# Optimization experiments

Measured on AMD Instinct MI355X. Metric: run time of the kernel, lower is better.

The kernel has to match this reference:

```python
import jax, jax.numpy as jnp
import numpy as np

N_NODES = 30000
N_EDGES = 480000
N_GRAPHS = 500
D_IN = 78


def gcn_conv(x, W, b, src, dst, n_nodes):
    """PyG GCNConv: add self-loops, sym-normalize, linear then aggregate, bias after."""
    xw = x @ W  # [N, d_out]
    deg = jnp.zeros((n_nodes,), x.dtype).at[dst].add(1.0) + 1.0  # +1 self-loop
    dinv = jax.lax.rsqrt(deg)
    norm = dinv[src] * dinv[dst]  # [E]
    msg = xw[src] * norm[:, None]  # [E, d_out] edge gather
    out = jnp.zeros_like(xw).at[dst].add(msg)  # scatter-add to dst
    out = out + xw * (dinv * dinv)[:, None]  # self-loop contribution
    return out + b


def setup_inputs() -> dict:
    key = jax.random.key(0)
    ks = jax.random.split(key, 16)
    x = jax.random.normal(ks[0], (N_NODES, D_IN), dtype=jnp.float32)
    edge_index = jax.random.randint(ks[1], (2, N_EDGES), 0, N_NODES, dtype=jnp.int32)
    batch = jnp.sort(jax.random.randint(ks[2], (N_NODES,), 0, N_GRAPHS, dtype=jnp.int32))

    def lin(k, fi, fo):
        s = 1.0 / np.sqrt(fi)
        k1, k2 = jax.random.split(k)
        W = jax.random.uniform(k1, (fi, fo), jnp.float32, -s, s)
        b = jax.random.uniform(k2, (fo,), jnp.float32, -s, s)
        return W, b

    W1, b1 = lin(ks[3], D_IN, D_IN)
    W2, b2 = lin(ks[4], D_IN, D_IN * 2)
    W3, b3 = lin(ks[5], D_IN * 2, D_IN * 4)
    Wf1, bf1 = lin(ks[6], D_IN * 4, 1024)
    Wf2, bf2 = lin(ks[7], 1024, 128)
    return {"x": x, "edge_index": edge_index, "batch": batch,
            "W1": W1, "b1": b1, "W2": W2, "b2": b2, "W3": W3, "b3": b3,
            "Wf1": Wf1, "bf1": bf1, "Wf2": Wf2, "bf2": bf2}


def reference(x, edge_index, batch, W1, b1, W2, b2, W3, b3, Wf1, bf1, Wf2, bf2):
    src, dst = edge_index[0], edge_index[1]
    n = x.shape[0]
    h = jax.nn.relu(gcn_conv(x, W1, b1, src, dst, n))
    h = jax.nn.relu(gcn_conv(h, W2, b2, src, dst, n))
    h = jax.nn.relu(gcn_conv(h, W3, b3, src, dst, n))
    # global max pool over graphs
    pooled = jax.ops.segment_max(h, batch, num_segments=N_GRAPHS)  # [G, 312]
    pooled = jnp.where(jnp.isfinite(pooled), pooled, 0.0)  # guard empty segments
    out = jax.nn.relu(pooled @ Wf1 + bf1)
    out = out @ Wf2 + bf2  # dropout is identity in eval mode
    return out
```

## Files before the change

kernel.cpp:

```cpp
#include <hip/hip_runtime.h>

#define NODES  30000
#define EDGES  480000
#define GRAPHS 500
#define MPAD   30016
#define NB     118

typedef __bf16 bf16x8 __attribute__((ext_vector_type(8)));
typedef float  f32x4  __attribute__((ext_vector_type(4)));

__device__ __forceinline__ float4 f4add(float4 a, float4 b) {
    a.x += b.x; a.y += b.y; a.z += b.z; a.w += b.w; return a;
}

__device__ __forceinline__ void split_f32(float a, unsigned short& hi, unsigned short& lo) {
    unsigned int u = __float_as_uint(a);
    unsigned int rh = (u + 0x7fffu + ((u >> 16) & 1u)) & 0xffff0000u;
    hi = (unsigned short)(rh >> 16);
    float l = a - __uint_as_float(rh);
    unsigned int ul = __float_as_uint(l);
    lo = (unsigned short)((ul + 0x7fffu + ((ul >> 16) & 1u)) >> 16);
}

__device__ __forceinline__ void gload_lds16(const void* g, void* l) {
    __builtin_amdgcn_global_load_lds(
        (__attribute__((address_space(1))) void*)g,
        (__attribute__((address_space(3))) void*)l, 16, 0, 0);
}

__global__ void count_kernel(const int* __restrict__ dst, int* __restrict__ cnt, int E) {
    int i = blockIdx.x * blockDim.x + threadIdx.x;
    if (i < E) atomicAdd(&cnt[dst[i]], 1);
}

__global__ __launch_bounds__(256) void scan_bsum_kernel(const int* __restrict__ cnt,
                                                        int* __restrict__ bsum, int n) {
    __shared__ int buf[256];
    int t = threadIdx.x;
    int i = blockIdx.x * 256 + t;
    buf[t] = (i < n) ? cnt[i] : 0;
    __syncthreads();
    for (int ofs = 128; ofs > 0; ofs >>= 1) {
        if (t < ofs) buf[t] += buf[t + ofs];
        __syncthreads();
    }
    if (t == 0) bsum[blockIdx.x] = buf[0];
}

__global__ __launch_bounds__(128) void scan_top_kernel(const int* __restrict__ bsum,
                                                       int* __restrict__ boff) {
    __shared__ int buf[128];
    int t = threadIdx.x;
    int own = (t < NB) ? bsum[t] : 0;
    buf[t] = own;
    __syncthreads();
    for (int ofs = 1; ofs < 128; ofs <<= 1) {
        int v = (t >= ofs) ? buf[t - ofs] : 0;
        __syncthreads();
        buf[t] += v;
        __syncthreads();
    }
    if (t < NB) boff[t] = buf[t] - own;
}

__global__ __launch_bounds__(256) void scan_apply_kernel(const int* __restrict__ cnt,
                                                         const int* __restrict__ boff,
                                                         int* __restrict__ rowstart,
                                                         float* __restrict__ dinv, int n) {
    __shared__ int buf[256];
    int t = threadIdx.x;
    int i = blockIdx.x * 256 + t;
    int own = (i < n) ? cnt[i] : 0;
    buf[t] = own;
    __syncthreads();
    for (int ofs = 1; ofs < 256; ofs <<= 1) {
        int v = (t >= ofs) ? buf[t - ofs] : 0;
        __syncthreads();
        buf[t] += v;
        __syncthreads();
    }
    if (i < n) {
        rowstart[i] = boff[blockIdx.x] + buf[t] - own;
        dinv[i] = rsqrtf((float)own + 1.0f);
    }
}

__global__ void fill_kernel(const int* __restrict__ src, const int* __restrict__ dst,
                            const int* __restrict__ rowstart, int* __restrict__ cursor,
                            int* __restrict__ csr_src, int E) {
    int i = blockIdx.x * blockDim.x + threadIdx.x;
    if (i < E) {
        int d = dst[i];
        int pos = atomicAdd(&cursor[d], 1);
        csr_src[rowstart[d] + pos] = src[i];
    }
}

__global__ void prescale_kernel(const float* __restrict__ X, const float* __restrict__ dinv,
                                float* __restrict__ Xs, int total) {
    int i = blockIdx.x * blockDim.x + threadIdx.x;
    if (i < total) {
        int node = i / 80;
        int c = i - node * 80;
        Xs[i] = (c < 78) ? X[node * 78 + c] * dinv[node] : 0.0f;
    }
}

__global__ void wsplit_kernel(const float* __restrict__ W, unsigned short* __restrict__ hi,
                              unsigned short* __restrict__ lo, int K, int N, int Kp) {
    int n = blockIdx.x, k = threadIdx.x;
    float v = (n < N && k < K) ? W[(size_t)k * N + n] : 0.0f;
    unsigned short h, l;
    split_f32(v, h, l);
    hi[(size_t)n * Kp + k] = h;
    lo[(size_t)n * Kp + k] = l;
}

template <int DV, int KQ>
__global__ __launch_bounds__(256) void agg_split_v3(
    const float* __restrict__ Xs, const int* __restrict__ rowstart,
    const int* __restrict__ cnt, const int* __restrict__ csr_src,
    const float* __restrict__ dinv,
    unsigned short* __restrict__ ohi, unsigned short* __restrict__ olo)
{
    constexpr int EPI = 64 / DV;
    constexpr int Kp = KQ * 4;
    int node = blockIdx.x * 4 + (threadIdx.x >> 6);
    int lane = threadIdx.x & 63;
    int sub = lane / DV;
    int c4 = lane - sub * DV;
    const float4* X4 = (const float4*)Xs;

    float4 acc0 = {0.f, 0.f, 0.f, 0.f}, acc1 = {0.f, 0.f, 0.f, 0.f};
    float4 acc2 = {0.f, 0.f, 0.f, 0.f}, acc3 = {0.f, 0.f, 0.f, 0.f};
    int s = rowstart[node];
    int e = s + cnt[node];

    if (sub < EPI) {
        if (sub == 0) acc0 = X4[(size_t)node * DV + c4];
        int j = s;
        for (; j + 8 * EPI <= e; j += 8 * EPI) {
            int i0 = csr_src[j + sub],           i1 = csr_src[j + EPI + sub];
            int i2 = csr_src[j + 2 * EPI + sub], i3 = csr_src[j + 3 * EPI + sub];
            int i4 = csr_src[j + 4 * EPI + sub], i5 = csr_src[j + 5 * EPI + sub];
            int i6 = csr_src[j + 6 * EPI + sub], i7 = csr_src[j + 7 * EPI + sub];
            float4 x0 = X4[(size_t)i0 * DV + c4], x1 = X4[(size_t)i1 * DV + c4];
            float4 x2 = X4[(size_t)i2 * DV + c4], x3 = X4[(size_t)i3 * DV + c4];
            float4 x4 = X4[(size_t)i4 * DV + c4], x5 = X4[(size_t)i5 * DV + c4];
            float4 x6 = X4[(size_t)i6 * DV + c4], x7 = X4[(size_t)i7 * DV + c4];
            acc0 = f4add(acc0, x0); acc1 = f4add(acc1, x1);
            acc2 = f4add(acc2, x2); acc3 = f4add(acc3, x3);
            acc0 = f4add(acc0, x4); acc1 = f4add(acc1, x5);
            acc2 = f4add(acc2, x6); acc3 = f4add(acc3, x7);
        }
        for (; j + 4 * EPI <= e; j += 4 * EPI) {
            int i0 = csr_src[j + sub],           i1 = csr_src[j + EPI + sub];
            int i2 = csr_src[j + 2 * EPI + sub], i3 = csr_src[j + 3 * EPI + sub];
            float4 x0 = X4[(size_t)i0 * DV + c4], x1 = X4[(size_t)i1 * DV + c4];
            float4 x2 = X4[(size_t)i2 * DV + c4], x3 = X4[(size_t)i3 * DV + c4];
            acc0 = f4add(acc0, x0); acc1 = f4add(acc1, x1);
            acc2 = f4add(acc2, x2); acc3 = f4add(acc3, x3);
        }
        for (; j < e; j += EPI) {
            int jj = j + sub;
            if (jj < e) {
                int idx = csr_src[jj];
                acc0 = f4add(acc0, X4[(size_t)idx * DV + c4]);
            }
        }
    }
    float4 acc = f4add(f4add(acc0, acc1), f4add(acc2, acc3));

    if constexpr (EPI > 1) {
        float sx[EPI - 1], sy[EPI - 1], sz[EPI - 1], sw[EPI - 1];
        #pragma unroll
        for (int sft = 1; sft < EPI; sft++) {
            sx[sft - 1] = __shfl(acc.x, lane + sft * DV);
            sy[sft - 1] = __shfl(acc.y, lane + sft * DV);
            sz[sft - 1] = __shfl(acc.z, lane + sft * DV);
            sw[sft - 1] = __shfl(acc.w, lane + sft * DV);
        }
        #pragma unroll
        for (int sft = 1; sft < EPI; sft++) {
            acc.x += sx[sft - 1];
            acc.y += sy[sft - 1];
            acc.z += sz[sft - 1];
            acc.w += sw[sft - 1];
        }
    }

    if (lane < DV) {
        float di = dinv[node];
        ushort4 h4, l4;
        split_f32(acc.x * di, h4.x, l4.x);
        split_f32(acc.y * di, h4.y, l4.y);
        split_f32(acc.z * di, h4.z, l4.z);
        split_f32(acc.w * di, h4.w, l4.w);
        *(ushort4*)&ohi[(size_t)node * Kp + lane * 4] = h4;
        *(ushort4*)&olo[(size_t)node * Kp + lane * 4] = l4;
    } else if (lane < KQ) {
        ushort4 z = {0, 0, 0, 0};
        *(ushort4*)&ohi[(size_t)node * Kp + lane * 4] = z;
        *(ushort4*)&olo[(size_t)node * Kp + lane * 4] = z;
    }
}

template <int NCK>
__global__ __launch_bounds__(256) void mfma_gemm_v2(
    const unsigned short* __restrict__ Ahi, const unsigned short* __restrict__ Alo,
    const unsigned short* __restrict__ Bhi, const unsigned short* __restrict__ Blo,
    const float* __restrict__ bias, const float* __restrict__ scale,
    float* __restrict__ C, int M, int N, int Cstride, int nN, int do_relu)
{
    constexpr int Kp = NCK * 32;
    constexpr int CELLS = NCK * 256;
    extern __shared__ unsigned short smem[];
    unsigned short* sA = smem;
    unsigned short* sB = smem + 2 * CELLS * 8;

    int t = threadIdx.x;
    int wv = t >> 6, ln = t & 63;
    int q = ln >> 4, l16 = ln & 15;
    int wm = wv & 1, wn = wv >> 1;
    int m0 = blockIdx.x * 64;

    #pragma unroll
    for (int i = 0; i < 2 * NCK; i++) {
        int c = i * 256 + t;
        int plane = c / CELLS;
        int r = c - plane * CELLS;
        int ck = r >> 8, qq = (r >> 6) & 3, row = r & 63;
        const unsigned short* src = (plane ? Alo : Ahi) + (size_t)(m0 + row) * Kp + ck * 32 + qq * 8;
        gload_lds16(src, &sA[(size_t)c * 8]);
    }

    for (int nt = 0; nt < nN; nt++) {
        int n0 = nt * 64;
        if (nt > 0) __syncthreads();
        #pragma unroll
        for (int i = 0; i < 2 * NCK; i++) {
            int c = i * 256 + t;
            int plane = c / CELLS;
            int r = c - plane * CELLS;
            int ck = r >> 8, qq = (r >> 6) & 3, row = r & 63;
            const unsigned short* src = (plane ? Blo : Bhi) + (size_t)(n0 + row) * Kp + ck * 32 + qq * 8;
            gload_lds16(src, &sB[(size_t)c * 8]);
        }
        __syncthreads();

        f32x4 acc[2][2] = {};
        #pragma unroll
        for (int ck = 0; ck < NCK; ck++) {
            bf16x8 ah[2], al[2], bh[2], bl[2];
            #pragma unroll
            for (int i = 0; i < 2; i++) {
                int ra = wm * 32 + i * 16 + l16;
                int rb = wn * 32 + i * 16 + l16;
                ah[i] = *(const bf16x8*)&sA[(size_t)(((0 * NCK + ck) * 4 + q) * 64 + ra) * 8];
                al[i] = *(const bf16x8*)&sA[(size_t)(((1 * NCK + ck) * 4 + q) * 64 + ra) * 8];
                bh[i] = *(const bf16x8*)&sB[(size_t)(((0 * NCK + ck) * 4 + q) * 64 + rb) * 8];
                bl[i] = *(const bf16x8*)&sB[(size_t)(((1 * NCK + ck) * 4 + q) * 64 + rb) * 8];
            }
            #pragma unroll
            for (int i = 0; i < 2; i++)
                #pragma unroll
                for (int j = 0; j < 2; j++) {
                    acc[i][j] = __builtin_amdgcn_mfma_f32_16x16x32_bf16(ah[i], bh[j], acc[i][j], 0, 0, 0);
                    acc[i][j] = __builtin_amdgcn_mfma_f32_16x16x32_bf16(ah[i], bl[j], acc[i][j], 0, 0, 0);
                    acc[i][j] = __builtin_amdgcn_mfma_f32_16x16x32_bf16(al[i], bh[j], acc[i][j], 0, 0, 0);
                }
        }

        #pragma unroll
        for (int i = 0; i < 2; i++) {
            int rbase = m0 + wm * 32 + i * 16 + q * 4;
            #pragma unroll
            for (int j = 0; j < 2; j++) {
                int col = n0 + wn * 32 + j * 16 + l16;
                if (col >= Cstride) continue;
                float bv = (col < N) ? bias[col] : 0.0f;
                #pragma unroll
                for (int r = 0; r < 4; r++) {
                    int row = rbase + r;
                    if (row < M) {
                        float v = 0.0f;
                        if (col < N) {
                            v = acc[i][j][r] + bv;
                            if (do_relu) v = fmaxf(v, 0.0f);
                            if (scale) v *= scale[row];
                        }
                        C[(size_t)row * Cstride + col] = v;
                    }
                }
            }
        }
    }
}

__device__ inline int lower_bound_dev(const int* a, int n, int v) {
    int lo = 0, hi = n;
    while (lo < hi) { int mid = (lo + hi) >> 1; if (a[mid] < v) lo = mid + 1; else hi = mid; }
    return lo;
}

__global__ void pool_kernel(const float* __restrict__ H, const int* __restrict__ batch,
                            float* __restrict__ pooled, int n, int G) {
    int g = blockIdx.x;
    int t = threadIdx.x;
    int s = lower_bound_dev(batch, n, g);
    int e = lower_bound_dev(batch, n, g + 1);
    if (t >= 78) return;
    const float4* H4 = (const float4*)H;
    float4 m = {0.f, 0.f, 0.f, 0.f};
    for (int i = s; i < e; i++) {
        float4 v = H4[(size_t)i * 78 + t];
        m.x = fmaxf(m.x, v.x); m.y = fmaxf(m.y, v.y);
        m.z = fmaxf(m.z, v.z); m.w = fmaxf(m.w, v.w);
    }
    ((float4*)pooled)[(size_t)g * 78 + t] = m;
}

__global__ __launch_bounds__(256) void fc1_kernel(const float* __restrict__ pooled,
                                                  const float* __restrict__ Wf1,
                                                  const float* __restrict__ bf1,
                                                  float* __restrict__ f1buf) {
    __shared__ float pl[4][312];
    int cb = blockIdx.x, gb = blockIdx.y;
    int t = threadIdx.x;
    for (int i = t; i < 4 * 312; i += 256) {
        int g = i / 312, k = i - g * 312;
        pl[g][k] = pooled[(size_t)(gb * 4 + g) * 312 + k];
    }
    __syncthreads();
    int col = cb * 256 + t;
    float a0 = 0.f, a1 = 0.f, a2 = 0.f, a3 = 0.f;
    #pragma unroll 4
    for (int k = 0; k < 312; k++) {
        float w = Wf1[(size_t)k * 1024 + col];
        a0 += pl[0][k] * w; a1 += pl[1][k] * w; a2 += pl[2][k] * w; a3 += pl[3][k] * w;
    }
    float b = bf1[col];
    int g0 = gb * 4;
    f1buf[(size_t)g0 * 1024 + col]       = fmaxf(a0 + b, 0.f);
    f1buf[(size_t)(g0 + 1) * 1024 + col] = fmaxf(a1 + b, 0.f);
    f1buf[(size_t)(g0 + 2) * 1024 + col] = fmaxf(a2 + b, 0.f);
    f1buf[(size_t)(g0 + 3) * 1024 + col] = fmaxf(a3 + b, 0.f);
}

__global__ __launch_bounds__(256) void fc2_part_kernel(const float* __restrict__ f1buf,
                                                       const float* __restrict__ Wf2,
                                                       float* __restrict__ partial) {
    __shared__ float f1s[4][128];
    __shared__ float red[256][4];
    int kt = blockIdx.x;
    int gb = blockIdx.y;
    int t = threadIdx.x;
    int col = t & 127, ks = t >> 7;
    for (int i = t; i < 512; i += 256) {
        int g = i >> 7, k = i & 127;
        f1s[g][k] = f1buf[(size_t)(gb * 4 + g) * 1024 + kt * 128 + k];
    }
    __syncthreads();
    float a0 = 0.f, a1 = 0.f, a2 = 0.f, a3 = 0.f;
    const float* w2 = Wf2 + (size_t)(kt * 128 + ks * 64) * 128 + col;
    #pragma unroll 4
    for (int k = 0; k < 64; k++) {
        float w = w2[(size_t)k * 128];
        int kk = ks * 64 + k;
        a0 += f1s[0][kk] * w; a1 += f1s[1][kk] * w; a2 += f1s[2][kk] * w; a3 += f1s[3][kk] * w;
    }
    red[t][0] = a0; red[t][1] = a1; red[t][2] = a2; red[t][3] = a3;
    __syncthreads();
    if (t < 128) {
        #pragma unroll
        for (int g = 0; g < 4; g++)
            partial[((size_t)kt * GRAPHS + gb * 4 + g) * 128 + col] = red[t][g] + red[t + 128][g];
    }
}

__global__ void fc2_reduce_kernel(const float* __restrict__ partial, const float* __restrict__ bf2,
                                  float* __restrict__ out, int total) {
    int i = blockIdx.x * blockDim.x + threadIdx.x;
    if (i < total) {
        float s = bf2[i & 127];
        #pragma unroll
        for (int kt = 0; kt < 8; kt++) s += partial[(size_t)kt * total + i];
        out[i] = s;
    }
}

extern "C" void kernel_launch(void* const* d_in, const int* in_sizes, int n_in,
                              void* d_out, int out_size, void* d_ws, size_t ws_size,
                              hipStream_t stream) {
    const float* x    = (const float*)d_in[0];
    const int*   ei   = (const int*)d_in[1];
    const int*   batch= (const int*)d_in[2];
    const float* W1 = (const float*)d_in[3];  const float* b1  = (const float*)d_in[4];
    const float* W2 = (const float*)d_in[5];  const float* b2  = (const float*)d_in[6];
    const float* W3 = (const float*)d_in[7];  const float* b3  = (const float*)d_in[8];
    const float* Wf1= (const float*)d_in[9];  const float* bf1 = (const float*)d_in[10];
    const float* Wf2= (const float*)d_in[11]; const float* bf2 = (const float*)d_in[12];
    float* out = (float*)d_out;

    const int* srcp = ei;
    const int* dstp = ei + EDGES;

    char* p = (char*)d_ws;
    size_t o = 0;
    auto takeB = [&](size_t bytes) { char* q = p + o; o += (bytes + 255) & ~(size_t)255; return q; };
    int*   cnt      = (int*)takeB(NODES * 4);
    int*   cursor   = (int*)takeB(NODES * 4);
    int*   rowstart = (int*)takeB(NODES * 4);
    int*   bsum     = (int*)takeB(NB * 4);
    int*   boff     = (int*)takeB(NB * 4);
    float* dinv     = (float*)takeB(NODES * 4);
    int*   csr_src  = (int*)takeB(EDGES * 4);
    unsigned short* aggH = (unsigned short*)takeB((size_t)MPAD * 160 * 2);
    unsigned short* aggL = (unsigned short*)takeB((size_t)MPAD * 160 * 2);
    float* xs      = (float*)takeB((size_t)NODES * 80 * 4);
    float* hbuf    = (float*)takeB((size_t)NODES * 312 * 4);
    float* pooled  = (float*)takeB((size_t)GRAPHS * 312 * 4);
    float* f1buf   = (float*)takeB((size_t)GRAPHS * 1024 * 4);
    float* partial = (float*)takeB((size_t)8 * GRAPHS * 128 * 4);
    unsigned short* Wt1h = (unsigned short*)takeB(128 * 96 * 2);
    unsigned short* Wt1l = (unsigned short*)takeB(128 * 96 * 2);
    unsigned short* Wt2h = (unsigned short*)takeB(192 * 96 * 2);
    unsigned short* Wt2l = (unsigned short*)takeB(192 * 96 * 2);
    unsigned short* Wt3h = (unsigned short*)takeB(320 * 160 * 2);
    unsigned short* Wt3l = (unsigned short*)takeB(320 * 160 * 2);
    (void)ws_size;

    hipMemsetAsync(cnt, 0, NODES * sizeof(int), stream);
    hipMemsetAsync(cursor, 0, NODES * sizeof(int), stream);

    wsplit_kernel<<<128, 96, 0, stream>>>(W1, Wt1h, Wt1l, 78, 78, 96);
    wsplit_kernel<<<192, 96, 0, stream>>>(W2, Wt2h, Wt2l, 78, 156, 96);
    wsplit_kernel<<<320, 160, 0, stream>>>(W3, Wt3h, Wt3l, 156, 312, 160);

    count_kernel<<<(EDGES + 255) / 256, 256, 0, stream>>>(dstp, cnt, EDGES);
    scan_bsum_kernel<<<NB, 256, 0, stream>>>(cnt, bsum, NODES);
    scan_top_kernel<<<1, 128, 0, stream>>>(bsum, boff);
    scan_apply_kernel<<<NB, 256, 0, stream>>>(cnt, boff, rowstart, dinv, NODES);
    fill_kernel<<<(EDGES + 255) / 256, 256, 0, stream>>>(srcp, dstp, rowstart, cursor, csr_src, EDGES);

    const int NBLK = MPAD / 64;
    const int AGRID = NODES / 4;

    prescale_kernel<<<(NODES * 80 + 255) / 256, 256, 0, stream>>>(x, dinv, xs, NODES * 80);
    agg_split_v3<20, 24><<<AGRID, 256, 0, stream>>>(xs, rowstart, cnt, csr_src, dinv, aggH, aggL);
    mfma_gemm_v2<3><<<NBLK, 256, 3 * 16384, stream>>>(aggH, aggL, Wt1h, Wt1l, b1, dinv, hbuf,
                                                      NODES, 78, 80, 2, 1);
    agg_split_v3<20, 24><<<AGRID, 256, 0, stream>>>(hbuf, rowstart, cnt, csr_src, dinv, aggH, aggL);
    mfma_gemm_v2<3><<<NBLK, 256, 3 * 16384, stream>>>(aggH, aggL, Wt2h, Wt2l, b2, dinv, hbuf,
                                                      NODES, 156, 160, 3, 1);
    agg_split_v3<40, 40><<<AGRID, 256, 0, stream>>>(hbuf, rowstart, cnt, csr_src, dinv, aggH, aggL);
    mfma_gemm_v2<5><<<NBLK, 256, 5 * 16384, stream>>>(aggH, aggL, Wt3h, Wt3l, b3, nullptr, hbuf,
                                                      NODES, 312, 312, 5, 1);

    pool_kernel<<<GRAPHS, 128, 0, stream>>>(hbuf, batch, pooled, NODES, GRAPHS);
    fc1_kernel<<<dim3(4, GRAPHS / 4), 256, 0, stream>>>(pooled, Wf1, bf1, f1buf);
    fc2_part_kernel<<<dim3(8, GRAPHS / 4), 256, 0, stream>>>(f1buf, Wf2, partial);
    fc2_reduce_kernel<<<(GRAPHS * 128 + 255) / 256, 256, 0, stream>>>(partial, bf2, out, GRAPHS * 128);
}
```

Before: 377.1 us.

## Fuse neighbor aggregation into MFMA GEMM, staging split operands in LDS

Replaces the separate aggregation kernel and GEMM with one kernel per layer. Each block gathers and sums neighbor features for its 64 rows, splits them into bf16 hi/lo, and writes them directly into shared memory before the MFMA loop. This removes the global round trip for the intermediate split buffers and three launches. The cost is far fewer, large-LDS blocks doing the latency-bound gather, which lowers the parallelism available to hide memory latency; a second hidden buffer is added to avoid in-place overwrite.

Result: slower. 420.4 us (+11.5%).

```diff
diff --git a/kernel.cpp b/kernel.cpp
--- a/kernel.cpp
+++ b/kernel.cpp
@@ -116,102 +116,16 @@
     lo[(size_t)n * Kp + k] = l;
 }
 
-template <int DV, int KQ>
-__global__ __launch_bounds__(256) void agg_split_v3(
-    const float* __restrict__ Xs, const int* __restrict__ rowstart,
-    const int* __restrict__ cnt, const int* __restrict__ csr_src,
-    const float* __restrict__ dinv,
-    unsigned short* __restrict__ ohi, unsigned short* __restrict__ olo)
-{
-    constexpr int EPI = 64 / DV;
-    constexpr int Kp = KQ * 4;
-    int node = blockIdx.x * 4 + (threadIdx.x >> 6);
-    int lane = threadIdx.x & 63;
-    int sub = lane / DV;
-    int c4 = lane - sub * DV;
-    const float4* X4 = (const float4*)Xs;
-
-    float4 acc0 = {0.f, 0.f, 0.f, 0.f}, acc1 = {0.f, 0.f, 0.f, 0.f};
-    float4 acc2 = {0.f, 0.f, 0.f, 0.f}, acc3 = {0.f, 0.f, 0.f, 0.f};
-    int s = rowstart[node];
-    int e = s + cnt[node];
-
-    if (sub < EPI) {
-        if (sub == 0) acc0 = X4[(size_t)node * DV + c4];
-        int j = s;
-        for (; j + 8 * EPI <= e; j += 8 * EPI) {
-            int i0 = csr_src[j + sub],           i1 = csr_src[j + EPI + sub];
-            int i2 = csr_src[j + 2 * EPI + sub], i3 = csr_src[j + 3 * EPI + sub];
-            int i4 = csr_src[j + 4 * EPI + sub], i5 = csr_src[j + 5 * EPI + sub];
-            int i6 = csr_src[j + 6 * EPI + sub], i7 = csr_src[j + 7 * EPI + sub];
-            float4 x0 = X4[(size_t)i0 * DV + c4], x1 = X4[(size_t)i1 * DV + c4];
-            float4 x2 = X4[(size_t)i2 * DV + c4], x3 = X4[(size_t)i3 * DV + c4];
-            float4 x4 = X4[(size_t)i4 * DV + c4], x5 = X4[(size_t)i5 * DV + c4];
-            float4 x6 = X4[(size_t)i6 * DV + c4], x7 = X4[(size_t)i7 * DV + c4];
-            acc0 = f4add(acc0, x0); acc1 = f4add(acc1, x1);
-            acc2 = f4add(acc2, x2); acc3 = f4add(acc3, x3);
-            acc0 = f4add(acc0, x4); acc1 = f4add(acc1, x5);
-            acc2 = f4add(acc2, x6); acc3 = f4add(acc3, x7);
-        }
-        for (; j + 4 * EPI <= e; j += 4 * EPI) {
-            int i0 = csr_src[j + sub],           i1 = csr_src[j + EPI + sub];
-            int i2 = csr_src[j + 2 * EPI + sub], i3 = csr_src[j + 3 * EPI + sub];
-            float4 x0 = X4[(size_t)i0 * DV + c4], x1 = X4[(size_t)i1 * DV + c4];
-            float4 x2 = X4[(size_t)i2 * DV + c4], x3 = X4[(size_t)i3 * DV + c4];
-            acc0 = f4add(acc0, x0); acc1 = f4add(acc1, x1);
-            acc2 = f4add(acc2, x2); acc3 = f4add(acc3, x3);
-        }
-        for (; j < e; j += EPI) {
-            int jj = j + sub;
-            if (jj < e) {
-                int idx = csr_src[jj];
-                acc0 = f4add(acc0, X4[(size_t)idx * DV + c4]);
-            }
-        }
-    }
-    float4 acc = f4add(f4add(acc0, acc1), f4add(acc2, acc3));
-
-    if constexpr (EPI > 1) {
-        float sx[EPI - 1], sy[EPI - 1], sz[EPI - 1], sw[EPI - 1];
-        #pragma unroll
-        for (int sft = 1; sft < EPI; sft++) {
-            sx[sft - 1] = __shfl(acc.x, lane + sft * DV);
-            sy[sft - 1] = __shfl(acc.y, lane + sft * DV);
-            sz[sft - 1] = __shfl(acc.z, lane + sft * DV);
-            sw[sft - 1] = __shfl(acc.w, lane + sft * DV);
-        }
-        #pragma unroll
-        for (int sft = 1; sft < EPI; sft++) {
-            acc.x += sx[sft - 1];
-            acc.y += sy[sft - 1];
-            acc.z += sz[sft - 1];
-            acc.w += sw[sft - 1];
-        }
-    }
-
-    if (lane < DV) {
-        float di = dinv[node];
-        ushort4 h4, l4;
-        split_f32(acc.x * di, h4.x, l4.x);
-        split_f32(acc.y * di, h4.y, l4.y);
-        split_f32(acc.z * di, h4.z, l4.z);
-        split_f32(acc.w * di, h4.w, l4.w);
-        *(ushort4*)&ohi[(size_t)node * Kp + lane * 4] = h4;
-        *(ushort4*)&olo[(size_t)node * Kp + lane * 4] = l4;
-    } else if (lane < KQ) {
-        ushort4 z = {0, 0, 0, 0};
-        *(ushort4*)&ohi[(size_t)node * Kp + lane * 4] = z;
-        *(ushort4*)&olo[(size_t)node * Kp + lane * 4] = z;
-    }
-}
-
-template <int NCK>
-__global__ __launch_bounds__(256) void mfma_gemm_v2(
-    const unsigned short* __restrict__ Ahi, const unsigned short* __restrict__ Alo,
+template <int DV, int KQ, int NCK>
+__global__ __launch_bounds__(256) void fused_agg_gemm(
+    const float* __restrict__ Xs,
+    const int* __restrict__ rowstart, const int* __restrict__ cnt,
+    const int* __restrict__ csr_src, const float* __restrict__ dinv,
     const unsigned short* __restrict__ Bhi, const unsigned short* __restrict__ Blo,
     const float* __restrict__ bias, const float* __restrict__ scale,
     float* __restrict__ C, int M, int N, int Cstride, int nN, int do_relu)
 {
+    constexpr int EPI = 64 / DV;
     constexpr int Kp = NCK * 32;
     constexpr int CELLS = NCK * 256;
     extern __shared__ unsigned short smem[];
@@ -224,19 +138,8 @@
     int wm = wv & 1, wn = wv >> 1;
     int m0 = blockIdx.x * 64;
 
-    #pragma unroll
-    for (int i = 0; i < 2 * NCK; i++) {
-        int c = i * 256 + t;
-        int plane = c / CELLS;
-        int r = c - plane * CELLS;
-        int ck = r >> 8, qq = (r >> 6) & 3, row = r & 63;
-        const unsigned short* src = (plane ? Alo : Ahi) + (size_t)(m0 + row) * Kp + ck * 32 + qq * 8;
-        gload_lds16(src, &sA[(size_t)c * 8]);
-    }
-
-    for (int nt = 0; nt < nN; nt++) {
+    auto stageB = [&](int nt) {
         int n0 = nt * 64;
-        if (nt > 0) __syncthreads();
         #pragma unroll
         for (int i = 0; i < 2 * NCK; i++) {
             int c = i * 256 + t;
@@ -245,6 +148,96 @@
             int ck = r >> 8, qq = (r >> 6) & 3, row = r & 63;
             const unsigned short* src = (plane ? Blo : Bhi) + (size_t)(n0 + row) * Kp + ck * 32 + qq * 8;
             gload_lds16(src, &sB[(size_t)c * 8]);
+        }
+    };
+
+    stageB(0);
+
+    {
+        int sub = ln / DV;
+        int c4 = ln - sub * DV;
+        const float4* X4 = (const float4*)Xs;
+        #pragma unroll 1
+        for (int it = 0; it < 16; it++) {
+            int row = wv * 16 + it;
+            int node = m0 + row;
+            bool valid = node < M;
+            float4 acc0 = {0.f, 0.f, 0.f, 0.f}, acc1 = acc0, acc2 = acc0, acc3 = acc0;
+            if (valid && sub < EPI) {
+                if (sub == 0) acc0 = X4[(size_t)node * DV + c4];
+                int s = rowstart[node];
+                int e = s + cnt[node];
+                int j = s;
+                for (; j + 8 * EPI <= e; j += 8 * EPI) {
+                    int i0 = csr_src[j + sub],           i1 = csr_src[j + EPI + sub];
+                    int i2 = csr_src[j + 2 * EPI + sub], i3 = csr_src[j + 3 * EPI + sub];
+                    int i4 = csr_src[j + 4 * EPI + sub], i5 = csr_src[j + 5 * EPI + sub];
+                    int i6 = csr_src[j + 6 * EPI + sub], i7 = csr_src[j + 7 * EPI + sub];
+                    float4 x0 = X4[(size_t)i0 * DV + c4], x1 = X4[(size_t)i1 * DV + c4];
+                    float4 x2 = X4[(size_t)i2 * DV + c4], x3 = X4[(size_t)i3 * DV + c4];
+                    float4 x4 = X4[(size_t)i4 * DV + c4], x5 = X4[(size_t)i5 * DV + c4];
+                    float4 x6 = X4[(size_t)i6 * DV + c4], x7 = X4[(size_t)i7 * DV + c4];
+                    acc0 = f4add(acc0, x0); acc1 = f4add(acc1, x1);
+                    acc2 = f4add(acc2, x2); acc3 = f4add(acc3, x3);
+                    acc0 = f4add(acc0, x4); acc1 = f4add(acc1, x5);
+                    acc2 = f4add(acc2, x6); acc3 = f4add(acc3, x7);
+                }
+                for (; j + 4 * EPI <= e; j += 4 * EPI) {
+                    int i0 = csr_src[j + sub],           i1 = csr_src[j + EPI + sub];
+                    int i2 = csr_src[j + 2 * EPI + sub], i3 = csr_src[j + 3 * EPI + sub];
+                    float4 x0 = X4[(size_t)i0 * DV + c4], x1 = X4[(size_t)i1 * DV + c4];
+                    float4 x2 = X4[(size_t)i2 * DV + c4], x3 = X4[(size_t)i3 * DV + c4];
+                    acc0 = f4add(acc0, x0); acc1 = f4add(acc1, x1);
+                    acc2 = f4add(acc2, x2); acc3 = f4add(acc3, x3);
+                }
+                for (; j < e; j += EPI) {
+                    int jj = j + sub;
+                    if (jj < e) {
+                        int idx = csr_src[jj];
+                        acc0 = f4add(acc0, X4[(size_t)idx * DV + c4]);
+                    }
+                }
+            }
+            float4 acc = f4add(f4add(acc0, acc1), f4add(acc2, acc3));
+
+            if constexpr (EPI > 1) {
+                float sx[EPI - 1], sy[EPI - 1], sz[EPI - 1], sw[EPI - 1];
+                #pragma unroll
+                for (int sft = 1; sft < EPI; sft++) {
+                    sx[sft - 1] = __shfl(acc.x, ln + sft * DV);
+                    sy[sft - 1] = __shfl(acc.y, ln + sft * DV);
+                    sz[sft - 1] = __shfl(acc.z, ln + sft * DV);
+                    sw[sft - 1] = __shfl(acc.w, ln + sft * DV);
+                }
+                #pragma unroll
+                for (int sft = 1; sft < EPI; sft++) {
+                    acc.x += sx[sft - 1];
+                    acc.y += sy[sft - 1];
+                    acc.z += sz[sft - 1];
+                    acc.w += sw[sft - 1];
+                }
+            }
+
+            if (ln < KQ) {
+                float di = (ln < DV && valid) ? dinv[node] : 0.0f;
+                ushort4 h4, l4;
+                split_f32(acc.x * di, h4.x, l4.x);
+                split_f32(acc.y * di, h4.y, l4.y);
+                split_f32(acc.z * di, h4.z, l4.z);
+                split_f32(acc.w * di, h4.w, l4.w);
+                int ck = ln >> 3, qq = (ln >> 1) & 3, ofs = (ln & 1) * 4;
+                size_t base = ((size_t)((ck * 4 + qq) * 64 + row)) * 8 + ofs;
+                *(ushort4*)&sA[base] = h4;
+                *(ushort4*)&sA[base + (size_t)CELLS * 8] = l4;
+            }
+        }
+    }
+
+    for (int nt = 0; nt < nN; nt++) {
+        int n0 = nt * 64;
+        if (nt > 0) {
+            __syncthreads();
+            stageB(nt);
         }
         __syncthreads();
 
@@ -415,10 +408,9 @@
     int*   boff     = (int*)takeB(NB * 4);
     float* dinv     = (float*)takeB(NODES * 4);
     int*   csr_src  = (int*)takeB(EDGES * 4);
-    unsigned short* aggH = (unsigned short*)takeB((size_t)MPAD * 160 * 2);
-    unsigned short* aggL = (unsigned short*)takeB((size_t)MPAD * 160 * 2);
-    float* xs      = (float*)takeB((size_t)NODES * 80 * 4);
-    float* hbuf    = (float*)takeB((size_t)NODES * 312 * 4);
+    float* xs      = (float*)takeB((size_t)MPAD * 80 * 4);
+    float* hbuf    = (float*)takeB((size_t)MPAD * 312 * 4);
+    float* hbuf2   = (float*)takeB((size_t)MPAD * 160 * 4);
     float* pooled  = (float*)takeB((size_t)GRAPHS * 312 * 4);
     float* f1buf   = (float*)takeB((size_t)GRAPHS * 1024 * 4);
     float* partial = (float*)takeB((size_t)8 * GRAPHS * 128 * 4);
@@ -444,18 +436,17 @@
     fill_kernel<<<(EDGES + 255) / 256, 256, 0, stream>>>(srcp, dstp, rowstart, cursor, csr_src, EDGES);
 
     const int NBLK = MPAD / 64;
-    const int AGRID = NODES / 4;
 
     prescale_kernel<<<(NODES * 80 + 255) / 256, 256, 0, stream>>>(x, dinv, xs, NODES * 80);
-    agg_split_v3<20, 24><<<AGRID, 256, 0, stream>>>(xs, rowstart, cnt, csr_src, dinv, aggH, aggL);
-    mfma_gemm_v2<3><<<NBLK, 256, 3 * 16384, stream>>>(aggH, aggL, Wt1h, Wt1l, b1, dinv, hbuf,
-                                                      NODES, 78, 80, 2, 1);
-    agg_split_v3<20, 24><<<AGRID, 256, 0, stream>>>(hbuf, rowstart, cnt, csr_src, dinv, aggH, aggL);
-    mfma_gemm_v2<3><<<NBLK, 256, 3 * 16384, stream>>>(aggH, aggL, Wt2h, Wt2l, b2, dinv, hbuf,
-                                                      NODES, 156, 160, 3, 1);
-    agg_split_v3<40, 40><<<AGRID, 256, 0, stream>>>(hbuf, rowstart, cnt, csr_src, dinv, aggH, aggL);
-    mfma_gemm_v2<5><<<NBLK, 256, 5 * 16384, stream>>>(aggH, aggL, Wt3h, Wt3l, b3, nullptr, hbuf,
-                                                      NODES, 312, 312, 5, 1);
+    fused_agg_gemm<20, 24, 3><<<NBLK, 256, 3 * 16384, stream>>>(
+        xs, rowstart, cnt, csr_src, dinv, Wt1h, Wt1l, b1, dinv, hbuf,
+        NODES, 78, 80, 2, 1);
+    fused_agg_gemm<20, 24, 3><<<NBLK, 256, 3 * 16384, stream>>>(
+        hbuf, rowstart, cnt, csr_src, dinv, Wt2h, Wt2l, b2, dinv, hbuf2,
+        NODES, 156, 160, 3, 1);
+    fused_agg_gemm<40, 40, 5><<<NBLK, 256, 5 * 16384, stream>>>(
+        hbuf2, rowstart, cnt, csr_src, dinv, Wt3h, Wt3l, b3, nullptr, hbuf,
+        NODES, 312, 312, 5, 1);
 
     pool_kernel<<<GRAPHS, 128, 0, stream>>>(hbuf, batch, pooled, NODES, GRAPHS);
     fc1_kernel<<<dim3(4, GRAPHS / 4), 256, 0, stream>>>(pooled, Wf1, bf1, f1buf);
```

## Fuse preprocessing and head kernels to cut launch count

Applied to the files above, without the earlier changes.

Merges the three weight-split launches with the degree count into one kernel, replaces the three-stage scan with a single 1024-thread block scan that also resets the cursor, and fuses CSR fill with input prescaling. On the output side, pooling is fused with fc1 (one block per 4 graphs, 6 row groups reducing in parallel), and fc2 is done in one kernel without partial buffers. This removes about eight launches and some intermediate traffic. In exchange, the fc1 and fc2 head kernels now run on only 125 blocks each, and the single-block scan is serial work.

Measured after the change: 411.0 us. 9.0% more time.

```diff
diff --git a/kernel.cpp b/kernel.cpp
--- a/kernel.cpp
+++ b/kernel.cpp
@@ -4,13 +4,16 @@
 #define EDGES  480000
 #define GRAPHS 500
 #define MPAD   30016
-#define NB     118
 
 typedef __bf16 bf16x8 __attribute__((ext_vector_type(8)));
 typedef float  f32x4  __attribute__((ext_vector_type(4)));
 
 __device__ __forceinline__ float4 f4add(float4 a, float4 b) {
     a.x += b.x; a.y += b.y; a.z += b.z; a.w += b.w; return a;
+}
+__device__ __forceinline__ float4 f4max(float4 a, float4 b) {
+    a.x = fmaxf(a.x, b.x); a.y = fmaxf(a.y, b.y);
+    a.z = fmaxf(a.z, b.z); a.w = fmaxf(a.w, b.w); return a;
 }
 
 __device__ __forceinline__ void split_f32(float a, unsigned short& hi, unsigned short& lo) {
@@ -28,96 +31,93 @@
         (__attribute__((address_space(3))) void*)l, 16, 0, 0);
 }
 
-__global__ void count_kernel(const int* __restrict__ dst, int* __restrict__ cnt, int E) {
-    int i = blockIdx.x * blockDim.x + threadIdx.x;
-    if (i < E) atomicAdd(&cnt[dst[i]], 1);
-}
-
-__global__ __launch_bounds__(256) void scan_bsum_kernel(const int* __restrict__ cnt,
-                                                        int* __restrict__ bsum, int n) {
-    __shared__ int buf[256];
+__global__ __launch_bounds__(256) void prep_kernel(
+    const float* __restrict__ W1, const float* __restrict__ W2, const float* __restrict__ W3,
+    unsigned short* __restrict__ h1, unsigned short* __restrict__ l1,
+    unsigned short* __restrict__ h2, unsigned short* __restrict__ l2,
+    unsigned short* __restrict__ h3, unsigned short* __restrict__ l3,
+    const int* __restrict__ dst, int* __restrict__ cnt)
+{
+    int b = blockIdx.x, t = threadIdx.x;
+    if (b < 640) {
+        const float* W; unsigned short *oh, *ol; int n, K, N, Kp;
+        if (b < 128)      { W = W1; oh = h1; ol = l1; n = b;       K = 78;  N = 78;  Kp = 96;  }
+        else if (b < 320) { W = W2; oh = h2; ol = l2; n = b - 128; K = 78;  N = 156; Kp = 96;  }
+        else              { W = W3; oh = h3; ol = l3; n = b - 320; K = 156; N = 312; Kp = 160; }
+        if (t < Kp) {
+            float v = (n < N && t < K) ? W[(size_t)t * N + n] : 0.0f;
+            unsigned short h, l;
+            split_f32(v, h, l);
+            oh[(size_t)n * Kp + t] = h;
+            ol[(size_t)n * Kp + t] = l;
+        }
+    } else {
+        int i = (b - 640) * 256 + t;
+        if (i < EDGES) atomicAdd(&cnt[dst[i]], 1);
+    }
+}
+
+__global__ __launch_bounds__(1024) void scan_single_kernel(
+    const int* __restrict__ cnt, int* __restrict__ rowstart,
+    int* __restrict__ cursor, float* __restrict__ dinv)
+{
+    __shared__ int sums[1024];
     int t = threadIdx.x;
-    int i = blockIdx.x * 256 + t;
-    buf[t] = (i < n) ? cnt[i] : 0;
+    int base = t * 30;
+    int c[30];
+    int s = 0;
+    #pragma unroll
+    for (int i = 0; i < 30; i++) {
+        int idx = base + i;
+        c[i] = (idx < NODES) ? cnt[idx] : 0;
+        s += c[i];
+    }
+    sums[t] = s;
     __syncthreads();
-    for (int ofs = 128; ofs > 0; ofs >>= 1) {
-        if (t < ofs) buf[t] += buf[t + ofs];
+    for (int ofs = 1; ofs < 1024; ofs <<= 1) {
+        int v = (t >= ofs) ? sums[t - ofs] : 0;
         __syncthreads();
-    }
-    if (t == 0) bsum[blockIdx.x] = buf[0];
-}
-
-__global__ __launch_bounds__(128) void scan_top_kernel(const int* __restrict__ bsum,
-                                                       int* __restrict__ boff) {
-    __shared__ int buf[128];
-    int t = threadIdx.x;
-    int own = (t < NB) ? bsum[t] : 0;
-    buf[t] = own;
-    __syncthreads();
-    for (int ofs = 1; ofs < 128; ofs <<= 1) {
-        int v = (t >= ofs) ? buf[t - ofs] : 0;
+        sums[t] += v;
         __syncthreads();
-        buf[t] += v;
-        __syncthreads();
-    }
-    if (t < NB) boff[t] = buf[t] - own;
-}
-
-__global__ __launch_bounds__(256) void scan_apply_kernel(const int* __restrict__ cnt,
-                                                         const int* __restrict__ boff,
-                                                         int* __restrict__ rowstart,
-                                                         float* __restrict__ dinv, int n) {
-    __shared__ int buf[256];
-    int t = threadIdx.x;
-    int i = blockIdx.x * 256 + t;
-    int own = (i < n) ? cnt[i] : 0;
-    buf[t] = own;
-    __syncthreads();
-    for (int ofs = 1; ofs < 256; ofs <<= 1) {
-        int v = (t >= ofs) ? buf[t - ofs] : 0;
-        __syncthreads();
-        buf[t] += v;
-        __syncthreads();
-    }
-    if (i < n) {
-        rowstart[i] = boff[blockIdx.x] + buf[t] - own;
-        dinv[i] = rsqrtf((float)own + 1.0f);
-    }
-}
-
-__global__ void fill_kernel(const int* __restrict__ src, const int* __restrict__ dst,
-                            const int* __restrict__ rowstart, int* __restrict__ cursor,
-                            int* __restrict__ csr_src, int E) {
-    int i = blockIdx.x * blockDim.x + threadIdx.x;
-    if (i < E) {
-        int d = dst[i];
-        int pos = atomicAdd(&cursor[d], 1);
-        csr_src[rowstart[d] + pos] = src[i];
-    }
-}
-
-__global__ void prescale_kernel(const float* __restrict__ X, const float* __restrict__ dinv,
-                                float* __restrict__ Xs, int total) {
-    int i = blockIdx.x * blockDim.x + threadIdx.x;
-    if (i < total) {
-        int node = i / 80;
-        int c = i - node * 80;
-        Xs[i] = (c < 78) ? X[node * 78 + c] * dinv[node] : 0.0f;
-    }
-}
-
-__global__ void wsplit_kernel(const float* __restrict__ W, unsigned short* __restrict__ hi,
-                              unsigned short* __restrict__ lo, int K, int N, int Kp) {
-    int n = blockIdx.x, k = threadIdx.x;
-    float v = (n < N && k < K) ? W[(size_t)k * N + n] : 0.0f;
-    unsigned short h, l;
-    split_f32(v, h, l);
-    hi[(size_t)n * Kp + k] = h;
-    lo[(size_t)n * Kp + k] = l;
+    }
+    int run = sums[t] - s;
+    #pragma unroll
+    for (int i = 0; i < 30; i++) {
+        int idx = base + i;
+        if (idx < NODES) {
+            rowstart[idx] = run;
+            cursor[idx] = 0;
+            dinv[idx] = rsqrtf((float)c[i] + 1.0f);
+            run += c[i];
+        }
+    }
+}
+
+__global__ __launch_bounds__(256) void fill_prescale_kernel(
+    const int* __restrict__ src, const int* __restrict__ dst,
+    const int* __restrict__ rowstart, int* __restrict__ cursor, int* __restrict__ csr_src,
+    const float* __restrict__ X, const float* __restrict__ dinv, float* __restrict__ Xs)
+{
+    int b = blockIdx.x, t = threadIdx.x;
+    if (b < 1875) {
+        int i = b * 256 + t;
+        if (i < EDGES) {
+            int d = dst[i];
+            int pos = atomicAdd(&cursor[d], 1);
+            csr_src[rowstart[d] + pos] = src[i];
+        }
+    } else {
+        int i = (b - 1875) * 256 + t;
+        if (i < NODES * 80) {
+            int node = i / 80;
+            int c = i - node * 80;
+            Xs[i] = (c < 78) ? X[node * 78 + c] * dinv[node] : 0.0f;
+        }
+    }
 }
 
 template <int DV, int KQ>
-__global__ __launch_bounds__(256) void agg_split_v3(
+__global__ __launch_bounds__(256) void agg_split_v4(
     const float* __restrict__ Xs, const int* __restrict__ rowstart,
     const int* __restrict__ cnt, const int* __restrict__ csr_src,
     const float* __restrict__ dinv,
@@ -189,19 +189,16 @@
         }
     }
 
-    if (lane < DV) {
-        float di = dinv[node];
+    if (lane < KQ) {
+        float di = (lane < DV) ? dinv[node] : 0.0f;
         ushort4 h4, l4;
         split_f32(acc.x * di, h4.x, l4.x);
         split_f32(acc.y * di, h4.y, l4.y);
         split_f32(acc.z * di, h4.z, l4.z);
         split_f32(acc.w * di, h4.w, l4.w);
-        *(ushort4*)&ohi[(size_t)node * Kp + lane * 4] = h4;
-        *(ushort4*)&olo[(size_t)node * Kp + lane * 4] = l4;
-    } else if (lane < KQ) {
-        ushort4 z = {0, 0, 0, 0};
-        *(ushort4*)&ohi[(size_t)node * Kp + lane * 4] = z;
-        *(ushort4*)&olo[(size_t)node * Kp + lane * 4] = z;
+        size_t off = (size_t)node * Kp + (size_t)lane * 4;
+        *(ushort4*)&ohi[off] = h4;
+        *(ushort4*)&olo[off] = l4;
     }
 }
 
@@ -303,89 +300,95 @@
     return lo;
 }
 
-__global__ void pool_kernel(const float* __restrict__ H, const int* __restrict__ batch,
-                            float* __restrict__ pooled, int n, int G) {
-    int g = blockIdx.x;
+__global__ __launch_bounds__(512) void pool_fc1_kernel(
+    const float* __restrict__ H, const int* __restrict__ batch,
+    const float* __restrict__ Wf1, const float* __restrict__ bf1,
+    float* __restrict__ f1buf)
+{
+    __shared__ float pl[4][312];
+    __shared__ float4 red[6][78];
+    int gb = blockIdx.x;
     int t = threadIdx.x;
-    int s = lower_bound_dev(batch, n, g);
-    int e = lower_bound_dev(batch, n, g + 1);
-    if (t >= 78) return;
+    int rg = t / 78, c = t - rg * 78;
     const float4* H4 = (const float4*)H;
-    float4 m = {0.f, 0.f, 0.f, 0.f};
-    for (int i = s; i < e; i++) {
-        float4 v = H4[(size_t)i * 78 + t];
-        m.x = fmaxf(m.x, v.x); m.y = fmaxf(m.y, v.y);
-        m.z = fmaxf(m.z, v.z); m.w = fmaxf(m.w, v.w);
-    }
-    ((float4*)pooled)[(size_t)g * 78 + t] = m;
-}
-
-__global__ __launch_bounds__(256) void fc1_kernel(const float* __restrict__ pooled,
-                                                  const float* __restrict__ Wf1,
-                                                  const float* __restrict__ bf1,
-                                                  float* __restrict__ f1buf) {
-    __shared__ float pl[4][312];
-    int cb = blockIdx.x, gb = blockIdx.y;
-    int t = threadIdx.x;
-    for (int i = t; i < 4 * 312; i += 256) {
-        int g = i / 312, k = i - g * 312;
-        pl[g][k] = pooled[(size_t)(gb * 4 + g) * 312 + k];
-    }
-    __syncthreads();
-    int col = cb * 256 + t;
-    float a0 = 0.f, a1 = 0.f, a2 = 0.f, a3 = 0.f;
+    for (int g = 0; g < 4; g++) {
+        int gg = gb * 4 + g;
+        int s = lower_bound_dev(batch, NODES, gg);
+        int e = lower_bound_dev(batch, NODES, gg + 1);
+        if (rg < 6) {
+            float4 m = {0.f, 0.f, 0.f, 0.f};
+            for (int i = s + rg; i < e; i += 6)
+                m = f4max(m, H4[(size_t)i * 78 + c]);
+            red[rg][c] = m;
+        }
+        __syncthreads();
+        if (t < 78) {
+            float4 m = red[0][t];
+            #pragma unroll
+            for (int r = 1; r < 6; r++) m = f4max(m, red[r][t]);
+            *(float4*)&pl[g][t * 4] = m;
+        }
+        __syncthreads();
+    }
+    int col = t * 2;
+    float a00 = 0.f, a01 = 0.f, a10 = 0.f, a11 = 0.f;
+    float a20 = 0.f, a21 = 0.f, a30 = 0.f, a31 = 0.f;
     #pragma unroll 4
     for (int k = 0; k < 312; k++) {
-        float w = Wf1[(size_t)k * 1024 + col];
-        a0 += pl[0][k] * w; a1 += pl[1][k] * w; a2 += pl[2][k] * w; a3 += pl[3][k] * w;
-    }
-    float b = bf1[col];
+        float2 w = *(const float2*)&Wf1[(size_t)k * 1024 + col];
+        float p0 = pl[0][k], p1 = pl[1][k], p2 = pl[2][k], p3 = pl[3][k];
+        a00 += p0 * w.x; a01 += p0 * w.y;
+        a10 += p1 * w.x; a11 += p1 * w.y;
+        a20 += p2 * w.x; a21 += p2 * w.y;
+        a30 += p3 * w.x; a31 += p3 * w.y;
+    }
+    float bx = bf1[col], by = bf1[col + 1];
     int g0 = gb * 4;
-    f1buf[(size_t)g0 * 1024 + col]       = fmaxf(a0 + b, 0.f);
-    f1buf[(size_t)(g0 + 1) * 1024 + col] = fmaxf(a1 + b, 0.f);
-    f1buf[(size_t)(g0 + 2) * 1024 + col] = fmaxf(a2 + b, 0.f);
-    f1buf[(size_t)(g0 + 3) * 1024 + col] = fmaxf(a3 + b, 0.f);
-}
-
-__global__ __launch_bounds__(256) void fc2_part_kernel(const float* __restrict__ f1buf,
-                                                       const float* __restrict__ Wf2,
-                                                       float* __restrict__ partial) {
-    __shared__ float f1s[4][128];
-    __shared__ float red[256][4];
-    int kt = blockIdx.x;
-    int gb = blockIdx.y;
+    float2 o0 = { fmaxf(a00 + bx, 0.f), fmaxf(a01 + by, 0.f) };
+    float2 o1 = { fmaxf(a10 + bx, 0.f), fmaxf(a11 + by, 0.f) };
+    float2 o2 = { fmaxf(a20 + bx, 0.f), fmaxf(a21 + by, 0.f) };
+    float2 o3 = { fmaxf(a30 + bx, 0.f), fmaxf(a31 + by, 0.f) };
+    *(float2*)&f1buf[(size_t)g0 * 1024 + col]       = o0;
+    *(float2*)&f1buf[(size_t)(g0 + 1) * 1024 + col] = o1;
+    *(float2*)&f1buf[(size_t)(g0 + 2) * 1024 + col] = o2;
+    *(float2*)&f1buf[(size_t)(g0 + 3) * 1024 + col] = o3;
+}
+
+__global__ __launch_bounds__(512) void fc2_kernel(
+    const float* __restrict__ f1buf, const float* __restrict__ Wf2,
+    const float* __restrict__ bf2, float* __restrict__ out)
+{
+    __shared__ float f1s[4][1024];
+    __shared__ float red[4][128][4];
+    int gb = blockIdx.x;
     int t = threadIdx.x;
+    const float4* F4 = (const float4*)(f1buf + (size_t)gb * 4 * 1024);
+    #pragma unroll
+    for (int i = 0; i < 2; i++) {
+        int idx = i * 512 + t;
+        ((float4*)f1s)[idx] = F4[idx];
+    }
+    __syncthreads();
     int col = t & 127, ks = t >> 7;
-    for (int i = t; i < 512; i += 256) {
-        int g = i >> 7, k = i & 127;
-        f1s[g][k] = f1buf[(size_t)(gb * 4 + g) * 1024 + kt * 128 + k];
-    }
-    __syncthreads();
     float a0 = 0.f, a1 = 0.f, a2 = 0.f, a3 = 0.f;
-    const float* w2 = Wf2 + (size_t)(kt * 128 + ks * 64) * 128 + col;
+    const float* w2 = Wf2 + (size_t)(ks * 256) * 128 + col;
     #pragma unroll 4
-    for (int k = 0; k < 64; k++) {
+    for (int k = 0; k < 256; k++) {
         float w = w2[(size_t)k * 128];
-        int kk = ks * 64 + k;
-        a0 += f1s[0][kk] * w; a1 += f1s[1][kk] * w; a2 += f1s[2][kk] * w; a3 += f1s[3][kk] * w;
-    }
-    red[t][0] = a0; red[t][1] = a1; red[t][2] = a2; red[t][3] = a3;
+        int kk = ks * 256 + k;
+        a0 += f1s[0][kk] * w; a1 += f1s[1][kk] * w;
+        a2 += f1s[2][kk] * w; a3 += f1s[3][kk] * w;
+    }
+    red[ks][col][0] = a0; red[ks][col][1] = a1;
+    red[ks][col][2] = a2; red[ks][col][3] = a3;
     __syncthreads();
     if (t < 128) {
-        #pragma unroll
-        for (int g = 0; g < 4; g++)
-            partial[((size_t)kt * GRAPHS + gb * 4 + g) * 128 + col] = red[t][g] + red[t + 128][g];
-    }
-}
-
-__global__ void fc2_reduce_kernel(const float* __restrict__ partial, const float* __restrict__ bf2,
-                                  float* __restrict__ out, int total) {
-    int i = blockIdx.x * blockDim.x + threadIdx.x;
-    if (i < total) {
-        float s = bf2[i & 127];
-        #pragma unroll
-        for (int kt = 0; kt < 8; kt++) s += partial[(size_t)kt * total + i];
-        out[i] = s;
+        float b = bf2[t];
+        #pragma unroll
+        for (int g = 0; g < 4; g++) {
+            float s = b + red[0][t][g] + red[1][t][g] + red[2][t][g] + red[3][t][g];
+            out[(size_t)(gb * 4 + g) * 128 + t] = s;
+        }
     }
 }
 
@@ -411,17 +414,13 @@
     int*   cnt      = (int*)takeB(NODES * 4);
     int*   cursor   = (int*)takeB(NODES * 4);
     int*   rowstart = (int*)takeB(NODES * 4);
-    int*   bsum     = (int*)takeB(NB * 4);
-    int*   boff     = (int*)takeB(NB * 4);
     float* dinv     = (float*)takeB(NODES * 4);
     int*   csr_src  = (int*)takeB(EDGES * 4);
     unsigned short* aggH = (unsigned short*)takeB((size_t)MPAD * 160 * 2);
     unsigned short* aggL = (unsigned short*)takeB((size_t)MPAD * 160 * 2);
     float* xs      = (float*)takeB((size_t)NODES * 80 * 4);
     float* hbuf    = (float*)takeB((size_t)NODES * 312 * 4);
-    float* pooled  = (float*)takeB((size_t)GRAPHS * 312 * 4);
     float* f1buf   = (float*)takeB((size_t)GRAPHS * 1024 * 4);
-    float* partial = (float*)takeB((size_t)8 * GRAPHS * 128 * 4);
     unsigned short* Wt1h = (unsigned short*)takeB(128 * 96 * 2);
     unsigned short* Wt1l = (unsigned short*)takeB(128 * 96 * 2);
     unsigned short* Wt2h = (unsigned short*)takeB(192 * 96 * 2);
@@ -431,34 +430,26 @@
     (void)ws_size;
 
     hipMemsetAsync(cnt, 0, NODES * sizeof(int), stream);
-    hipMemsetAsync(cursor, 0, NODES * sizeof(int), stream);
-
-    wsplit_kernel<<<128, 96, 0, stream>>>(W1, Wt1h, Wt1l, 78, 78, 96);
-    wsplit_kernel<<<192, 96, 0, stream>>>(W2, Wt2h, Wt2l, 78, 156, 96);
-    wsplit_kernel<<<320, 160, 0, stream>>>(W3, Wt3h, Wt3l, 156, 312, 160);
-
-    count_kernel<<<(EDGES + 255) / 256, 256, 0, stream>>>(dstp, cnt, EDGES);
-    scan_bsum_kernel<<<NB, 256, 0, stream>>>(cnt, bsum, NODES);
-    scan_top_kernel<<<1, 128, 0, stream>>>(bsum, boff);
-    scan_apply_kernel<<<NB, 256, 0, stream>>>(cnt, boff, rowstart, dinv, NODES);
-    fill_kernel<<<(EDGES + 255) / 256, 256, 0, stream>>>(srcp, dstp, rowstart, cursor, csr_src, EDGES);
+
+    prep_kernel<<<640 + 1875, 256, 0, stream>>>(W1, W2, W3, Wt1h, Wt1l, Wt2h, Wt2l,
+                                                Wt3h, Wt3l, dstp, cnt);
+    scan_single_kernel<<<1, 1024, 0, stream>>>(cnt, rowstart, cursor, dinv);
+    fill_prescale_kernel<<<1875 + 9375, 256, 0, stream>>>(srcp, dstp, rowstart, cursor,
+                                                          csr_src, x, dinv, xs);
 
     const int NBLK = MPAD / 64;
     const int AGRID = NODES / 4;
 
-    prescale_kernel<<<(NODES * 80 + 255) / 256, 256, 0, stream>>>(x, dinv, xs, NODES * 80);
-    agg_split_v3<20, 24><<<AGRID, 256, 0, stream>>>(xs, rowstart, cnt, csr_src, dinv, aggH, aggL);
+    agg_split_v4<20, 24><<<AGRID, 256, 0, stream>>>(xs, rowstart, cnt, csr_src, dinv, aggH, aggL);
     mfma_gemm_v2<3><<<NBLK, 256, 3 * 16384, stream>>>(aggH, aggL, Wt1h, Wt1l, b1, dinv, hbuf,
                                                       NODES, 78, 80, 2, 1);
-    agg_split_v3<20, 24><<<AGRID, 256, 0, stream>>>(hbuf, rowstart, cnt, csr_src, dinv, aggH, aggL);
+    agg_split_v4<20, 24><<<AGRID, 256, 0, stream>>>(hbuf, rowstart, cnt, csr_src, dinv, aggH, aggL);
     mfma_gemm_v2<3><<<NBLK, 256, 3 * 16384, stream>>>(aggH, aggL, Wt2h, Wt2l, b2, dinv, hbuf,
                                                       NODES, 156, 160, 3, 1);
-    agg_split_v3<40, 40><<<AGRID, 256, 0, stream>>>(hbuf, rowstart, cnt, csr_src, dinv, aggH, aggL);
+    agg_split_v4<40, 40><<<AGRID, 256, 0, stream>>>(hbuf, rowstart, cnt, csr_src, dinv, aggH, aggL);
     mfma_gemm_v2<5><<<NBLK, 256, 5 * 16384, stream>>>(aggH, aggL, Wt3h, Wt3l, b3, nullptr, hbuf,
                                                       NODES, 312, 312, 5, 1);
 
-    pool_kernel<<<GRAPHS, 128, 0, stream>>>(hbuf, batch, pooled, NODES, GRAPHS);
-    fc1_kernel<<<dim3(4, GRAPHS / 4), 256, 0, stream>>>(pooled, Wf1, bf1, f1buf);
-    fc2_part_kernel<<<dim3(8, GRAPHS / 4), 256, 0, stream>>>(f1buf, Wf2, partial);
-    fc2_reduce_kernel<<<(GRAPHS * 128 + 255) / 256, 256, 0, stream>>>(partial, bf2, out, GRAPHS * 128);
-}
+    pool_fc1_kernel<<<GRAPHS / 4, 512, 0, stream>>>(hbuf, batch, Wf1, bf1, f1buf);
+    fc2_kernel<<<GRAPHS / 4, 512, 0, stream>>>(f1buf, Wf2, bf2, out);
+}
```
